# Kernel tuning notes

Measured on AMD Instinct MI355X. Metric: run time of the kernel, lower is better.

Reference implementation:

```python
import jax, jax.numpy as jnp
import numpy as np

B, N0, NCLS = 8, 1024, 40
SPACING, SIGMA_FACTOR = 2.0, 1.0
BLOCKS = [[64, 64], [128, 128], [256, 1024]]
POOL_SIZES = [256, 64, 1]
FC1, FC2 = 512, 256
# 3x3x3 kernel translation grid (27-point support, hard-coded in ConvLayer)
GRID = jnp.asarray(np.array([[i, j, k] for i in (-1, 0, 1) for j in (-1, 0, 1) for k in (-1, 0, 1)], dtype=np.float32))  # [27,3]


def pcnn_conv(pc, feat, W, b, sigma):
    """Extension-operator point convolution.
    pc [B,N,3], feat [B,N,Cin], W [27,Cin,Cout], b [Cout].
    out[b,i,o] = relu( (1/N) * sum_l sum_j exp(-||p_i - p_j + t_l||^2/(2 ks^2)) f[b,j] @ W[l] + b )
    """
    ks = SIGMA_FACTOR * sigma
    trans = SPACING * sigma * GRID                      # [27,3]
    inv = 1.0 / (2.0 * ks * ks)
    diff = pc[:, :, None, :] - pc[:, None, :, :]        # [B,N,N,3]
    d2 = jnp.sum(diff * diff, -1)                       # [B,N,N]
    n = pc.shape[1]

    def body(acc, wt):
        t, Wl = wt                                      # t [3], Wl [Cin,Cout]
        # ||diff + t||^2 = d2 + 2 diff.t + |t|^2
        e = jnp.exp(-(d2 + 2.0 * jnp.einsum('bijd,d->bij', diff, t) + jnp.dot(t, t)) * inv)
        s = jnp.einsum('bij,bjc->bic', e, feat)         # Gaussian-weighted gather
        return acc + jnp.einsum('bic,co->bio', s, Wl), None

    out0 = jnp.zeros((pc.shape[0], n, W.shape[2]), feat.dtype)
    out, _ = jax.lax.scan(body, out0, (trans, W))
    return jax.nn.relu(out / n + b)


def fps(pts, m):
    """Farthest point sampling. pts [N,3] -> indices [m]."""
    d = jnp.sum((pts - pts[0]) ** 2, -1)
    idxs = jnp.zeros((m,), jnp.int32)

    def body(i, state):
        idxs, d = state
        nxt = jnp.argmax(d).astype(jnp.int32)
        idxs = idxs.at[i].set(nxt)
        d = jnp.minimum(d, jnp.sum((pts - pts[nxt]) ** 2, -1))
        return idxs, d

    idxs, _ = jax.lax.fori_loop(1, m, body, (idxs, d))
    return idxs


def pool(pc, feat, m):
    """FPS subsample to m centers, max-pool features over nearest-center clusters."""
    idx = jax.vmap(lambda p: fps(p, m))(pc)                      # [B,m]
    centers = jnp.take_along_axis(pc, idx[..., None], axis=1)    # [B,m,3]
    dist = jnp.sum((pc[:, :, None, :] - centers[:, None, :, :]) ** 2, -1)  # [B,N,m]
    assign = jnp.argmin(dist, -1)                                # [B,N]
    pooled = jax.vmap(lambda f, a: jax.ops.segment_max(f, a, num_segments=m))(feat, assign)
    return centers, pooled


def bn(x, g, b):
    mu = jnp.mean(x, 0)
    v = jnp.var(x, 0)
    return g * (x - mu) * jax.lax.rsqrt(v + 1e-5) + b


def setup_inputs() -> dict:
    key = jax.random.key(0)
    ks = jax.random.split(key, 24)
    inp = {"pc": jax.random.normal(ks[0], (B, 3, N0), jnp.float32)}
    chans = [4, 64, 64, 128, 128, 256, 1024]
    for i, (ci, co) in enumerate(zip(chans[:-1], chans[1:])):
        inp[f"w_c{i}"] = jax.random.normal(ks[1 + i], (27, ci, co), jnp.float32) * 0.05
        inp[f"b_c{i}"] = jnp.zeros((co,), jnp.float32)
    inp["w_fc1"] = jax.random.normal(ks[10], (1024, FC1), jnp.float32) * 0.03
    inp["g_fc1"] = jnp.ones((FC1,), jnp.float32)
    inp["be_fc1"] = jnp.zeros((FC1,), jnp.float32)
    inp["w_fc2"] = jax.random.normal(ks[11], (FC1, FC2), jnp.float32) * 0.05
    inp["g_fc2"] = jnp.ones((FC2,), jnp.float32)
    inp["be_fc2"] = jnp.zeros((FC2,), jnp.float32)
    inp["w_fc3"] = jax.random.normal(ks[12], (FC2, NCLS), jnp.float32) * 0.05
    inp["b_fc3"] = jnp.zeros((NCLS,), jnp.float32)
    return inp


def reference(pc, w_c0, b_c0, w_c1, b_c1, w_c2, b_c2, w_c3, b_c3, w_c4, b_c4, w_c5, b_c5,
              w_fc1, g_fc1, be_fc1, w_fc2, g_fc2, be_fc2, w_fc3, b_fc3):
    pts = jnp.transpose(pc, (0, 2, 1))                           # [B,N,3]
    b_, n0, _ = pts.shape
    feat = jnp.concatenate([pts, jnp.ones((b_, n0, 1), pts.dtype)], -1)  # [B,N,4]
    sigma = 1.0 / float(np.sqrt(n0))  # faithfully uses initial N for all blocks
    ws = [(w_c0, b_c0), (w_c1, b_c1), (w_c2, b_c2), (w_c3, b_c3), (w_c4, b_c4), (w_c5, b_c5)]
    idx = 0
    cur = pts
    for bi, block in enumerate(BLOCKS):
        for _ in block:
            W, bb = ws[idx]
            feat = pcnn_conv(cur, feat, W, bb, sigma)
            idx += 1
        cur, feat = pool(cur, feat, POOL_SIZES[bi])
    x = feat.reshape(b_, -1)                                     # [B,1024]
    x = jax.nn.relu(bn(x @ w_fc1, g_fc1, be_fc1))
    x = jax.nn.relu(bn(x @ w_fc2, g_fc2, be_fc2))
    return x @ w_fc3 + b_fc3
```

## Files before the change

kernel.cpp:

```cpp
#include <hip/hip_runtime.h>
#include <cstdint>
#include <cstddef>
#include <cmath>

constexpr int B = 8;
constexpr int N0 = 1024;
constexpr int CAP = 64;
using u16 = unsigned short;

typedef __bf16 bf16x8 __attribute__((ext_vector_type(8)));
typedef float f32x4 __attribute__((ext_vector_type(4)));

__device__ inline u16 f2bf(float x) {
  unsigned u = __float_as_uint(x);
  return (u16)((u + 0x7fffu + ((u >> 16) & 1u)) >> 16);
}
__device__ inline float bf2f(u16 h) { return __uint_as_float(((unsigned)h) << 16); }
__device__ inline int swk2(int row, int k) {
  int s = (((row >> 2) ^ (row >> 4)) & 3);
  return ((((k >> 3) ^ s) << 3) | (k & 7));
}

__global__ __launch_bounds__(256) void k_prep(const float* __restrict__ pc,
                                              float* __restrict__ pts,
                                              float* __restrict__ feat0,
                                              uint4* __restrict__ p3, int n3,
                                              uint4* __restrict__ p6, int n6,
                                              uint4* __restrict__ p9, int n9) {
  int idx = blockIdx.x * blockDim.x + threadIdx.x;
  if (idx < B * N0) {
    int b = idx / N0, i = idx - b * N0;
    float x = pc[(b * 3 + 0) * N0 + i];
    float y = pc[(b * 3 + 1) * N0 + i];
    float z = pc[(b * 3 + 2) * N0 + i];
    pts[idx * 3 + 0] = x; pts[idx * 3 + 1] = y; pts[idx * 3 + 2] = z;
    feat0[idx * 4 + 0] = x; feat0[idx * 4 + 1] = y; feat0[idx * 4 + 2] = z; feat0[idx * 4 + 3] = 1.0f;
  }
  uint4 v = make_uint4(0xFFFFFFFFu, 0xFFFFFFFFu, 0xFFFFFFFFu, 0xFFFFFFFFu);
  for (int i = idx; i < n3; i += B * N0) p3[i] = v;
  for (int i = idx; i < n6; i += B * N0) p6[i] = v;
  for (int i = idx; i < n9; i += B * N0) p9[i] = v;
}

__global__ __launch_bounds__(256) void k_pairs(const float* __restrict__ pts,
                                               int* __restrict__ pidx, int* __restrict__ pcnt,
                                               int N) {
  const int r = blockIdx.x * 4 + (threadIdx.x >> 6);
  const int lane = threadIdx.x & 63;
  const int b = r / N;
  const float px = pts[(size_t)r * 3 + 0];
  const float py = pts[(size_t)r * 3 + 1];
  const float pz = pts[(size_t)r * 3 + 2];
  int* row = pidx + (size_t)r * CAP;
  int base = 0;
  for (int j0 = 0; j0 < N; j0 += 64) {
    int j = j0 + lane;
    float dx = px - pts[((size_t)b * N + j) * 3 + 0];
    float dy = py - pts[((size_t)b * N + j) * 3 + 1];
    float dz = pz - pts[((size_t)b * N + j) * 3 + 2];
    float d2 = dx * dx + dy * dy + dz * dz;
    bool keep = d2 <= 0.1228f;
    unsigned long long mk = __ballot(keep);
    int pos = __popcll(mk & ((1ull << lane) - 1ull));
    if (keep) { int s = base + pos; if (s < CAP) row[s] = j; }
    base += __popcll(mk);
  }
  if (lane == 0) pcnt[r] = base < CAP ? base : CAP;
}

__global__ void k_econtract(const float* __restrict__ pts, const float* __restrict__ feat,
                            const int* __restrict__ pidx, const int* __restrict__ pcnt,
                            u16* __restrict__ Shi, u16* __restrict__ Slo,
                            int N, int Cin, int K, int Kpad, int mbase) {
  const int g = mbase + blockIdx.x;
  const int b = g / N;
  const int t = threadIdx.x;
  const bool cact = t < Cin;
  const float px = pts[(size_t)g * 3 + 0];
  const float py = pts[(size_t)g * 3 + 1];
  const float pz = pts[(size_t)g * 3 + 2];
  float acc[27];
#pragma unroll
  for (int l = 0; l < 27; ++l) acc[l] = 0.f;
  const int n = pcnt[g];
  const int* row = pidx + (size_t)g * CAP;
  for (int p = 0; p < n; ++p) {
    int j = row[p];
    size_t jb = (size_t)b * N + j;
    float dx = px - pts[jb * 3 + 0];
    float dy = py - pts[jb * 3 + 1];
    float dz = pz - pts[jb * 3 + 2];
    float d2 = dx * dx + dy * dy + dz * dz;
    float base_ = __expf(-512.f * d2);
    float gxv[3] = {__expf(64.f * dx - 2.f), 1.f, __expf(-64.f * dx - 2.f)};
    float gyv[3] = {__expf(64.f * dy - 2.f), 1.f, __expf(-64.f * dy - 2.f)};
    float gzv[3] = {__expf(64.f * dz - 2.f), 1.f, __expf(-64.f * dz - 2.f)};
    float fv = cact ? feat[jb * Cin + t] : 0.f;
#pragma unroll
    for (int a = 0; a < 3; ++a) {
      float ba = base_ * gxv[a];
#pragma unroll
      for (int b2 = 0; b2 < 3; ++b2) {
        float bab = ba * gyv[b2];
#pragma unroll
        for (int c2 = 0; c2 < 3; ++c2) {
          int l = a * 9 + b2 * 3 + c2;
          acc[l] = fmaf(bab * gzv[c2], fv, acc[l]);
        }
      }
    }
  }
  size_t rowo = (size_t)blockIdx.x * Kpad;
  if (cact) {
#pragma unroll
    for (int l = 0; l < 27; ++l) {
      float v = acc[l];
      u16 h = f2bf(v);
      u16 lo = f2bf(v - bf2f(h));
      Shi[rowo + (size_t)l * Cin + t] = h;
      Slo[rowo + (size_t)l * Cin + t] = lo;
    }
  }
  if (Kpad > K && t >= Cin && t < Cin + (Kpad - K)) {
    size_t po = rowo + K + (t - Cin);
    Shi[po] = 0; Slo[po] = 0;
  }
}

__global__ __launch_bounds__(512) void k_gemm_mfma(const u16* __restrict__ Shi,
                                                   const u16* __restrict__ Slo,
                                                   const float* __restrict__ W,
                                                   const float* __restrict__ bias,
                                                   float* __restrict__ out,
                                                   float* __restrict__ P,
                                                   int K, int Kpad, int Cout, float scale,
                                                   int mcur) {
  __shared__ u16 As[2][2][32][40];
  __shared__ u16 Bs[2][2][64][40];
  __shared__ float xch[4][64][8];
  const int t = threadIdx.x;
  const int h = t >> 8;
  const int tl = t & 255;
  const int nb = blockIdx.x * 64;
  const int m0 = blockIdx.y * 32;
  const int l = t & 63, w = t >> 6;
  const int ks = w >> 2, wq = w & 3;
  const int wm = (wq >> 1) * 16, wn = (wq & 1) * 32;
  const int la = l & 15, lg = l >> 4;
  const int ntiles = Kpad >> 6;
  const int KZ = gridDim.z, z = blockIdx.z;
  const int q = ntiles / KZ, r = ntiles % KZ;
  const int t0 = z * q + (z < r ? z : r);
  const int cnt = q + (z < r ? 1 : 0);
  const int ar = tl >> 3, ak = (tl & 7) * 4;
  const size_t aOff = (size_t)(m0 + ar) * Kpad + h * 32 + ak;
  const int aw = swk2(ar, ak);
  const int kp = (tl >> 4) * 2, n4 = (tl & 15) * 4;
  f32x4 acc0 = {0.f, 0.f, 0.f, 0.f}, acc1 = {0.f, 0.f, 0.f, 0.f};

  for (int kt = 0; kt < cnt; ++kt) {
    const int k0 = (t0 + kt) * 64;
    *(ushort4*)&As[h][0][ar][aw] = *(const ushort4*)(Shi + aOff + k0);
    *(ushort4*)&As[h][1][ar][aw] = *(const ushort4*)(Slo + aOff + k0);
    {
      int gk0 = k0 + h * 32 + kp;
      float4 b0 = make_float4(0.f, 0.f, 0.f, 0.f), b1 = b0;
      if (gk0 < K) b0 = *(const float4*)(W + (size_t)gk0 * Cout + nb + n4);
      if (gk0 + 1 < K) b1 = *(const float4*)(W + (size_t)(gk0 + 1) * Cout + nb + n4);
      float v0[4] = {b0.x, b0.y, b0.z, b0.w};
      float v1[4] = {b1.x, b1.y, b1.z, b1.w};
#pragma unroll
      for (int e = 0; e < 4; ++e) {
        int n = n4 + e;
        int kw = swk2(n, kp);
        u16 h0 = f2bf(v0[e]);
        u16 l0 = f2bf(v0[e] - bf2f(h0));
        u16 h1 = f2bf(v1[e]);
        u16 l1 = f2bf(v1[e] - bf2f(h1));
        *(unsigned*)&Bs[h][0][n][kw] = (unsigned)h0 | ((unsigned)h1 << 16);
        *(unsigned*)&Bs[h][1][n][kw] = (unsigned)l0 | ((unsigned)l1 << 16);
      }
    }
    __syncthreads();
    bf16x8 ah = *(const bf16x8*)&As[ks][0][wm + la][swk2(wm + la, lg * 8)];
    bf16x8 al = *(const bf16x8*)&As[ks][1][wm + la][swk2(wm + la, lg * 8)];
    bf16x8 bh0 = *(const bf16x8*)&Bs[ks][0][wn + la][swk2(wn + la, lg * 8)];
    bf16x8 bl0 = *(const bf16x8*)&Bs[ks][1][wn + la][swk2(wn + la, lg * 8)];
    bf16x8 bh1 = *(const bf16x8*)&Bs[ks][0][wn + 16 + la][swk2(wn + 16 + la, lg * 8)];
    bf16x8 bl1 = *(const bf16x8*)&Bs[ks][1][wn + 16 + la][swk2(wn + 16 + la, lg * 8)];
    acc0 = __builtin_amdgcn_mfma_f32_16x16x32_bf16(ah, bh0, acc0, 0, 0, 0);
    acc1 = __builtin_amdgcn_mfma_f32_16x16x32_bf16(ah, bh1, acc1, 0, 0, 0);
    acc0 = __builtin_amdgcn_mfma_f32_16x16x32_bf16(al, bh0, acc0, 0, 0, 0);
    acc1 = __builtin_amdgcn_mfma_f32_16x16x32_bf16(al, bh1, acc1, 0, 0, 0);
    acc0 = __builtin_amdgcn_mfma_f32_16x16x32_bf16(ah, bl0, acc0, 0, 0, 0);
    acc1 = __builtin_amdgcn_mfma_f32_16x16x32_bf16(ah, bl1, acc1, 0, 0, 0);
    __syncthreads();
  }
  if (w >= 4) {
#pragma unroll
    for (int r2 = 0; r2 < 4; ++r2) { xch[wq][l][r2] = acc0[r2]; xch[wq][l][r2 + 4] = acc1[r2]; }
  }
  __syncthreads();
  if (w < 4) {
#pragma unroll
    for (int r2 = 0; r2 < 4; ++r2) { acc0[r2] += xch[wq][l][r2]; acc1[r2] += xch[wq][l][r2 + 4]; }
    if (gridDim.z == 1) {
#pragma unroll
      for (int r2 = 0; r2 < 4; ++r2) {
        int gm = m0 + wm + lg * 4 + r2;
        int gn0 = nb + wn + la;
        out[(size_t)gm * Cout + gn0] = fmaxf(fmaf(acc0[r2], scale, bias[gn0]), 0.f);
        int gn1 = gn0 + 16;
        out[(size_t)gm * Cout + gn1] = fmaxf(fmaf(acc1[r2], scale, bias[gn1]), 0.f);
      }
    } else {
      float* Pz = P + (size_t)z * mcur * Cout;
#pragma unroll
      for (int r2 = 0; r2 < 4; ++r2) {
        int gm = m0 + wm + lg * 4 + r2;
        int gn0 = nb + wn + la;
        Pz[(size_t)gm * Cout + gn0] = acc0[r2];
        Pz[(size_t)gm * Cout + gn0 + 16] = acc1[r2];
      }
    }
  }
}

__global__ __launch_bounds__(256) void k_reduce(const float* __restrict__ P,
                                                const float* __restrict__ bias,
                                                float* __restrict__ out,
                                                int n4, int Cout, int KZ, float scale,
                                                int stride) {
  int i = blockIdx.x * 256 + threadIdx.x;
  if (i >= n4) return;
  float4 s = *(const float4*)(P + (size_t)i * 4);
  for (int z = 1; z < KZ; ++z) {
    float4 v = *(const float4*)(P + (size_t)z * stride + (size_t)i * 4);
    s.x += v.x; s.y += v.y; s.z += v.z; s.w += v.w;
  }
  int c = (i * 4) % Cout;
  float4 bb = *(const float4*)(bias + c);
  float4 o;
  o.x = fmaxf(fmaf(s.x, scale, bb.x), 0.f);
  o.y = fmaxf(fmaf(s.y, scale, bb.y), 0.f);
  o.z = fmaxf(fmaf(s.z, scale, bb.z), 0.f);
  o.w = fmaxf(fmaf(s.w, scale, bb.w), 0.f);
  *(float4*)(out + (size_t)i * 4) = o;
}

template <int CTRL>
__device__ __forceinline__ float dppmaxf(float v) {
  int o = __builtin_amdgcn_update_dpp(0, __float_as_int(v), CTRL, 0xF, 0xF, true);
  return fmaxf(v, __int_as_float(o));
}
__device__ __forceinline__ float wavemaxf(float v) {
  v = dppmaxf<0xB1>(v);
  v = dppmaxf<0x4E>(v);
  v = dppmaxf<0x141>(v);
  v = dppmaxf<0x140>(v);
  v = dppmaxf<0x142>(v);
  v = dppmaxf<0x143>(v);
  return __uint_as_float((unsigned)__builtin_amdgcn_readlane(__float_as_int(v), 63));
}

#define FPS_LOAD(i) \
  float qx##i = src[3 * i + 0], qy##i = src[3 * i + 1], qz##i = src[3 * i + 2];
#define FPS_D0(i) \
  float d##i; { float ax = __fsub_rn(qx##i, x0), ay = __fsub_rn(qy##i, y0), az = __fsub_rn(qz##i, z0); \
    d##i = __fadd_rn(__fadd_rn(__fmul_rn(ax, ax), __fmul_rn(ay, ay)), __fmul_rn(az, az)); }
#define FPS_UPD(i) \
  { float ax = __fsub_rn(qx##i, cx), ay = __fsub_rn(qy##i, cy), az = __fsub_rn(qz##i, cz); \
    float nd = __fadd_rn(__fadd_rn(__fmul_rn(ax, ax), __fmul_rn(ay, ay)), __fmul_rn(az, az)); \
    d##i = fminf(d##i, nd); }
#define FPS_SEL(i) \
  { bool e = (d##i == lbest); sx = e ? qx##i : sx; sy = e ? qy##i : sy; sz = e ? qz##i : sz; }

__global__ __launch_bounds__(64, 1) void k_fps1024(const float* __restrict__ pts,
                                                   float* __restrict__ centers, int m) {
  const int b = blockIdx.x;
  const int t = threadIdx.x;
  const float* P = pts + (size_t)b * 1024 * 3;
  const float* src = P + t * 16 * 3;
  FPS_LOAD(0) FPS_LOAD(1) FPS_LOAD(2) FPS_LOAD(3)
  FPS_LOAD(4) FPS_LOAD(5) FPS_LOAD(6) FPS_LOAD(7)
  FPS_LOAD(8) FPS_LOAD(9) FPS_LOAD(10) FPS_LOAD(11)
  FPS_LOAD(12) FPS_LOAD(13) FPS_LOAD(14) FPS_LOAD(15)
  float x0 = P[0], y0 = P[1], z0 = P[2];
  FPS_D0(0) FPS_D0(1) FPS_D0(2) FPS_D0(3)
  FPS_D0(4) FPS_D0(5) FPS_D0(6) FPS_D0(7)
  FPS_D0(8) FPS_D0(9) FPS_D0(10) FPS_D0(11)
  FPS_D0(12) FPS_D0(13) FPS_D0(14) FPS_D0(15)
  if (t == 0) {
    centers[(size_t)b * m * 3 + 0] = x0;
    centers[(size_t)b * m * 3 + 1] = y0;
    centers[(size_t)b * m * 3 + 2] = z0;
  }
  float lbest;
  {
    float a0 = fmaxf(d0, d1), a1 = fmaxf(d2, d3), a2 = fmaxf(d4, d5), a3 = fmaxf(d6, d7);
    float a4 = fmaxf(d8, d9), a5 = fmaxf(d10, d11), a6 = fmaxf(d12, d13), a7 = fmaxf(d14, d15);
    float b0 = fmaxf(a0, a1), b1 = fmaxf(a2, a3), b2 = fmaxf(a4, a5), b3 = fmaxf(a6, a7);
    lbest = fmaxf(fmaxf(b0, b1), fmaxf(b2, b3));
  }
  for (int it = 1; it < m; ++it) {
    float sx = qx15, sy = qy15, sz = qz15;
    FPS_SEL(14) FPS_SEL(13) FPS_SEL(12) FPS_SEL(11)
    FPS_SEL(10) FPS_SEL(9) FPS_SEL(8) FPS_SEL(7)
    FPS_SEL(6) FPS_SEL(5) FPS_SEL(4) FPS_SEL(3)
    FPS_SEL(2) FPS_SEL(1) FPS_SEL(0)
    float wmax = wavemaxf(lbest);
    unsigned long long mask = __ballot(lbest == wmax);
    int fl = __ffsll((long long)mask) - 1;
    float cx = __uint_as_float((unsigned)__builtin_amdgcn_readlane(__float_as_int(sx), fl));
    float cy = __uint_as_float((unsigned)__builtin_amdgcn_readlane(__float_as_int(sy), fl));
    float cz = __uint_as_float((unsigned)__builtin_amdgcn_readlane(__float_as_int(sz), fl));
    if (t == 0) {
      centers[((size_t)b * m + it) * 3 + 0] = cx;
      centers[((size_t)b * m + it) * 3 + 1] = cy;
      centers[((size_t)b * m + it) * 3 + 2] = cz;
    }
    FPS_UPD(0) FPS_UPD(1) FPS_UPD(2) FPS_UPD(3)
    FPS_UPD(4) FPS_UPD(5) FPS_UPD(6) FPS_UPD(7)
    FPS_UPD(8) FPS_UPD(9) FPS_UPD(10) FPS_UPD(11)
    FPS_UPD(12) FPS_UPD(13) FPS_UPD(14) FPS_UPD(15)
    {
      float a0 = fmaxf(d0, d1), a1 = fmaxf(d2, d3), a2 = fmaxf(d4, d5), a3 = fmaxf(d6, d7);
      float a4 = fmaxf(d8, d9), a5 = fmaxf(d10, d11), a6 = fmaxf(d12, d13), a7 = fmaxf(d14, d15);
      float b0 = fmaxf(a0, a1), b1 = fmaxf(a2, a3), b2 = fmaxf(a4, a5), b3 = fmaxf(a6, a7);
      lbest = fmaxf(fmaxf(b0, b1), fmaxf(b2, b3));
    }
  }
}

__global__ __launch_bounds__(64, 1) void k_fps256(const float* __restrict__ pts,
                                                  float* __restrict__ centers, int m) {
  const int b = blockIdx.x;
  const int t = threadIdx.x;
  const float* P = pts + (size_t)b * 256 * 3;
  const float* src = P + t * 4 * 3;
  FPS_LOAD(0) FPS_LOAD(1) FPS_LOAD(2) FPS_LOAD(3)
  float x0 = P[0], y0 = P[1], z0 = P[2];
  FPS_D0(0) FPS_D0(1) FPS_D0(2) FPS_D0(3)
  if (t == 0) {
    centers[(size_t)b * m * 3 + 0] = x0;
    centers[(size_t)b * m * 3 + 1] = y0;
    centers[(size_t)b * m * 3 + 2] = z0;
  }
  float lbest = fmaxf(fmaxf(d0, d1), fmaxf(d2, d3));
  for (int it = 1; it < m; ++it) {
    float sx = qx3, sy = qy3, sz = qz3;
    FPS_SEL(2) FPS_SEL(1) FPS_SEL(0)
    float wmax = wavemaxf(lbest);
    unsigned long long mask = __ballot(lbest == wmax);
    int fl = __ffsll((long long)mask) - 1;
    float cx = __uint_as_float((unsigned)__builtin_amdgcn_readlane(__float_as_int(sx), fl));
    float cy = __uint_as_float((unsigned)__builtin_amdgcn_readlane(__float_as_int(sy), fl));
    float cz = __uint_as_float((unsigned)__builtin_amdgcn_readlane(__float_as_int(sz), fl));
    if (t == 0) {
      centers[((size_t)b * m + it) * 3 + 0] = cx;
      centers[((size_t)b * m + it) * 3 + 1] = cy;
      centers[((size_t)b * m + it) * 3 + 2] = cz;
    }
    FPS_UPD(0) FPS_UPD(1) FPS_UPD(2) FPS_UPD(3)
    lbest = fmaxf(fmaxf(d0, d1), fmaxf(d2, d3));
  }
}

__global__ __launch_bounds__(64) void k_center0(const float* __restrict__ pts,
                                                float* __restrict__ centers,
                                                int* __restrict__ assign) {
  const int b = blockIdx.x, t = threadIdx.x;
  if (t < 3) centers[b * 3 + t] = pts[(size_t)b * 64 * 3 + t];
  assign[b * 64 + t] = 0;
}

__global__ __launch_bounds__(256) void k_assign(const float* __restrict__ pts,
                                                const float* __restrict__ centers,
                                                int* __restrict__ assign, int N, int m) {
  __shared__ float cs[256 * 3];
  const int t = threadIdx.x;
  const int idx = blockIdx.x * 256 + t;
  const int b = (blockIdx.x * 256) / N;
  for (int i = t; i < m * 3; i += 256) cs[i] = centers[(size_t)b * m * 3 + i];
  __syncthreads();
  float px = pts[(size_t)idx * 3 + 0], py = pts[(size_t)idx * 3 + 1], pz = pts[(size_t)idx * 3 + 2];
  float best = 3.4e38f; int bk = 0;
  for (int k = 0; k < m; ++k) {
    float dx = __fsub_rn(px, cs[k * 3 + 0]);
    float dy = __fsub_rn(py, cs[k * 3 + 1]);
    float dz = __fsub_rn(pz, cs[k * 3 + 2]);
    float dd = __fadd_rn(__fadd_rn(__fmul_rn(dx, dx), __fmul_rn(dy, dy)), __fmul_rn(dz, dz));
    if (dd < best) { best = dd; bk = k; }
  }
  assign[idx] = bk;
}

__global__ __launch_bounds__(256) void k_segmax(const float* __restrict__ feat,
                                                const int* __restrict__ assign,
                                                float* __restrict__ pooled,
                                                int N, int m, int C) {
  int idx = blockIdx.x * blockDim.x + threadIdx.x;
  if (idx >= B * N * C) return;
  int b = idx / (N * C);
  int r = idx - b * N * C;
  int i = r / C;
  int c = r - i * C;
  int a = assign[b * N + i];
  atomicMax((int*)&pooled[((size_t)b * m + a) * C + c], __float_as_int(feat[idx]));
}

template <int K, int COUT, bool BNR>
__global__ __launch_bounds__(256) void k_fc(const float* __restrict__ x,
                                            const float* __restrict__ w,
                                            const float* __restrict__ g,
                                            const float* __restrict__ be,
                                            float* __restrict__ out) {
  __shared__ float ys[8][33];
  int t = threadIdx.x;
  int n = t >> 5, cl = t & 31;
  int c = blockIdx.x * 32 + cl;
  float acc = 0.f;
  if (c < COUT) {
    const float* xr = x + n * K;
    float a0 = 0.f, a1 = 0.f, a2 = 0.f, a3 = 0.f;
    for (int k = 0; k < K; k += 4) {
      a0 = fmaf(xr[k + 0], w[(size_t)(k + 0) * COUT + c], a0);
      a1 = fmaf(xr[k + 1], w[(size_t)(k + 1) * COUT + c], a1);
      a2 = fmaf(xr[k + 2], w[(size_t)(k + 2) * COUT + c], a2);
      a3 = fmaf(xr[k + 3], w[(size_t)(k + 3) * COUT + c], a3);
    }
    acc = (a0 + a1) + (a2 + a3);
  }
  ys[n][cl] = acc;
  __syncthreads();
  if (c >= COUT) return;
  if (BNR) {
    float mu = 0.f;
#pragma unroll
    for (int q = 0; q < 8; ++q) mu += ys[q][cl];
    mu *= 0.125f;
    float var = 0.f;
#pragma unroll
    for (int q = 0; q < 8; ++q) { float dv = ys[q][cl] - mu; var = fmaf(dv, dv, var); }
    var *= 0.125f;
    float rs = 1.f / sqrtf(var + 1e-5f);
    float v = g[c] * (acc - mu) * rs + be[c];
    out[n * COUT + c] = fmaxf(v, 0.f);
  } else {
    out[n * COUT + c] = acc + be[c];
  }
}

extern "C" void kernel_launch(void* const* d_in, const int* in_sizes, int n_in,
                              void* d_out, int out_size, void* d_ws, size_t ws_size,
                              hipStream_t stream) {
  (void)in_sizes; (void)n_in; (void)out_size;
  const float* pc = (const float*)d_in[0];
  const float* Wc[6]; const float* bc[6];
  for (int l = 0; l < 6; ++l) { Wc[l] = (const float*)d_in[1 + 2 * l]; bc[l] = (const float*)d_in[2 + 2 * l]; }
  const float* w1 = (const float*)d_in[13];
  const float* g1 = (const float*)d_in[14];
  const float* be1 = (const float*)d_in[15];
  const float* w2 = (const float*)d_in[16];
  const float* g2 = (const float*)d_in[17];
  const float* be2 = (const float*)d_in[18];
  const float* w3 = (const float*)d_in[19];
  const float* b3 = (const float*)d_in[20];

  float* ws = (float*)d_ws;
  size_t o = 0;
  auto A = [&](size_t n) { size_t r = o; o += (n + 63) & ~(size_t)63; return r; };
  const size_t PTS0 = A((size_t)B * 1024 * 3);
  const size_t PTS1 = A((size_t)B * 256 * 3);
  const size_t PTS2 = A((size_t)B * 64 * 3);
  const size_t PTS3 = A((size_t)B * 3);
  const size_t F0  = A((size_t)B * 1024 * 4);
  const size_t FB1 = A((size_t)B * 1024 * 64);
  const size_t FB2 = A((size_t)B * 1024 * 64);
  const size_t FB3 = A((size_t)B * 256 * 64);
  const size_t FB4 = A((size_t)B * 256 * 128);
  const size_t FB5 = A((size_t)B * 256 * 128);
  const size_t FB6 = A((size_t)B * 64 * 128);
  const size_t FB7 = A((size_t)B * 64 * 256);
  const size_t FB8 = A((size_t)B * 64 * 1024);
  const size_t FB9 = A((size_t)B * 1024);
  const size_t ASSIGN = A((size_t)B * 1024);
  const size_t Y1 = A((size_t)8 * 512);
  const size_t Y2 = A((size_t)8 * 256);
  const size_t PIDX = A((size_t)B * 1024 * CAP);
  const size_t PCNT = A((size_t)B * 1024);
  const size_t dynB = o * sizeof(float);

  int* pidx = (int*)(ws + PIDX);
  int* pcnt = (int*)(ws + PCNT);

  k_prep<<<dim3((B * N0 + 255) / 256), dim3(256), 0, stream>>>(
      pc, ws + PTS0, ws + F0,
      (uint4*)(ws + FB3), B * 256 * 64 / 4,
      (uint4*)(ws + FB6), B * 64 * 128 / 4,
      (uint4*)(ws + FB9), B * 1024 / 4);

  auto conv = [&](size_t ptsOff, size_t finOff, size_t foutOff, int Npts, int Cin, int Cout,
                  const float* W, const float* bias) {
    const int M = B * Npts;
    const int K = 27 * Cin;
    const int Kpad = (K + 63) & ~63;
    const size_t availB = (ws_size > dynB) ? ws_size - dynB : 0;
    size_t pResB = availB / 4;
    if (pResB > (size_t)13 << 20) pResB = (size_t)13 << 20;
    const size_t sByte = availB - pResB;
    long mc = (long)(sByte / ((size_t)Kpad * 4)) & ~31L;
    int Mc = (int)((mc < (long)M) ? mc : (long)M);
    if (Mc < 32) Mc = 32;
    u16* Shi = (u16*)((char*)d_ws + dynB);
    u16* Slo = Shi + (size_t)Mc * Kpad;
    float* P = (float*)(Shi + (size_t)2 * Mc * Kpad);
    const int mch = (M + Mc - 1) / Mc;
    const float scale = 1.f / (float)Npts;
    const int blk = (Cin <= 64) ? 64 : Cin;
    const int ntiles = Kpad >> 6;
    for (int mcb = 0; mcb < mch; ++mcb) {
      const int mb0 = mcb * Mc;
      const int mcur = ((M - mb0) < Mc) ? (M - mb0) : Mc;
      k_econtract<<<dim3(mcur), dim3(blk), 0, stream>>>(ws + ptsOff, ws + finOff, pidx, pcnt,
                                                        Shi, Slo, Npts, Cin, K, Kpad, mb0);
      const int gx = Cout / 64, gy = mcur / 32;
      int kz = 1024 / (gx * gy);
      if (kz < 1) kz = 1;
      if (kz > ntiles) kz = ntiles;
      if (kz > 16) kz = 16;
      long pcap = (long)(pResB / ((size_t)mcur * Cout * 4));
      if ((long)kz > pcap) kz = (pcap < 1) ? 1 : (int)pcap;
      float* outp = ws + foutOff + (size_t)mb0 * Cout;
      k_gemm_mfma<<<dim3(gx, gy, kz), dim3(512), 0, stream>>>(
          Shi, Slo, W, bias, outp, P, K, Kpad, Cout, scale, mcur);
      if (kz > 1) {
        int n4 = mcur * Cout / 4;
        k_reduce<<<dim3((n4 + 255) / 256), dim3(256), 0, stream>>>(
            P, bias, outp, n4, Cout, kz, scale, mcur * Cout);
      }
    }
  };

  k_pairs<<<dim3(B * 1024 / 4), dim3(256), 0, stream>>>(ws + PTS0, pidx, pcnt, 1024);
  conv(PTS0, F0, FB1, 1024, 4, 64, Wc[0], bc[0]);
  conv(PTS0, FB1, FB2, 1024, 64, 64, Wc[1], bc[1]);
  k_fps1024<<<dim3(B), dim3(64), 0, stream>>>(ws + PTS0, ws + PTS1, 256);
  k_assign<<<dim3(B * 1024 / 256), dim3(256), 0, stream>>>(ws + PTS0, ws + PTS1, (int*)(ws + ASSIGN), 1024, 256);
  k_segmax<<<dim3((B * 1024 * 64 + 255) / 256), dim3(256), 0, stream>>>(ws + FB2, (int*)(ws + ASSIGN), ws + FB3, 1024, 256, 64);
  k_pairs<<<dim3(B * 256 / 4), dim3(256), 0, stream>>>(ws + PTS1, pidx, pcnt, 256);
  conv(PTS1, FB3, FB4, 256, 64, 128, Wc[2], bc[2]);
  conv(PTS1, FB4, FB5, 256, 128, 128, Wc[3], bc[3]);
  k_fps256<<<dim3(B), dim3(64), 0, stream>>>(ws + PTS1, ws + PTS2, 64);
  k_assign<<<dim3(B * 256 / 256), dim3(256), 0, stream>>>(ws + PTS1, ws + PTS2, (int*)(ws + ASSIGN), 256, 64);
  k_segmax<<<dim3((B * 256 * 128 + 255) / 256), dim3(256), 0, stream>>>(ws + FB5, (int*)(ws + ASSIGN), ws + FB6, 256, 64, 128);
  k_pairs<<<dim3(B * 64 / 4), dim3(256), 0, stream>>>(ws + PTS2, pidx, pcnt, 64);
  conv(PTS2, FB6, FB7, 64, 128, 256, Wc[4], bc[4]);
  conv(PTS2, FB7, FB8, 64, 256, 1024, Wc[5], bc[5]);
  k_center0<<<dim3(B), dim3(64), 0, stream>>>(ws + PTS2, ws + PTS3, (int*)(ws + ASSIGN));
  k_segmax<<<dim3((B * 64 * 1024 + 255) / 256), dim3(256), 0, stream>>>(ws + FB8, (int*)(ws + ASSIGN), ws + FB9, 64, 1, 1024);
  k_fc<1024, 512, true><<<dim3(512 / 32), dim3(256), 0, stream>>>(ws + FB9, w1, g1, be1, ws + Y1);
  k_fc<512, 256, true><<<dim3(256 / 32), dim3(256), 0, stream>>>(ws + Y1, w2, g2, be2, ws + Y2);
  k_fc<256, 40, false><<<dim3(2), dim3(256), 0, stream>>>(ws + Y2, w3, nullptr, b3, (float*)d_out);
}
```

Measured before the change: 437.8 us.

## Share per-neighbor Gaussian weights via LDS and pack FPS math into pk_f32 ops

In the extension-contraction kernel, lanes 0-26 of each wave now compute one of the 27 translated Gaussian weights directly with a single exp each. The weights go into shared memory, and every channel thread reads them back instead of recomputing 7 exps and the product tree per neighbor. The FPS kernels pair points into float2 vectors and use inline v_pk_add/v_pk_mul to halve the VALU instruction count of the distance update. The exp restructure changes rounding slightly. The LDS exchange relies on a wave-level waitcnt with no barrier, which is only correct because each wave uses its own slot.

```diff
diff --git a/kernel.cpp b/kernel.cpp
--- a/kernel.cpp
+++ b/kernel.cpp
@@ -10,6 +10,7 @@
 
 typedef __bf16 bf16x8 __attribute__((ext_vector_type(8)));
 typedef float f32x4 __attribute__((ext_vector_type(4)));
+typedef float f32x2 __attribute__((ext_vector_type(2)));
 
 __device__ inline u16 f2bf(float x) {
   unsigned u = __float_as_uint(x);
@@ -19,6 +20,12 @@
 __device__ inline int swk2(int row, int k) {
   int s = (((row >> 2) ^ (row >> 4)) & 3);
   return ((((k >> 3) ^ s) << 3) | (k & 7));
+}
+__device__ __forceinline__ f32x2 pkadd(f32x2 a, f32x2 b) {
+  f32x2 d; asm("v_pk_add_f32 %0, %1, %2" : "=v"(d) : "v"(a), "v"(b)); return d;
+}
+__device__ __forceinline__ f32x2 pkmul(f32x2 a, f32x2 b) {
+  f32x2 d; asm("v_pk_mul_f32 %0, %1, %2" : "=v"(d) : "v"(a), "v"(b)); return d;
 }
 
 __global__ __launch_bounds__(256) void k_prep(const float* __restrict__ pc,
@@ -72,13 +79,23 @@
                             const int* __restrict__ pidx, const int* __restrict__ pcnt,
                             u16* __restrict__ Shi, u16* __restrict__ Slo,
                             int N, int Cin, int K, int Kpad, int mbase) {
+  __shared__ float eL[4][28];
   const int g = mbase + blockIdx.x;
   const int b = g / N;
   const int t = threadIdx.x;
+  const int w = t >> 6, lane = t & 63;
   const bool cact = t < Cin;
   const float px = pts[(size_t)g * 3 + 0];
   const float py = pts[(size_t)g * 3 + 1];
   const float pz = pts[(size_t)g * 3 + 2];
+  float sxc = 0.f, syc = 0.f, szc = 0.f, cst = 0.f;
+  if (lane < 27) {
+    int a = lane / 9, bb = (lane / 3) % 3, cc = lane % 3;
+    sxc = (a == 0) ? 64.f : ((a == 2) ? -64.f : 0.f);
+    syc = (bb == 0) ? 64.f : ((bb == 2) ? -64.f : 0.f);
+    szc = (cc == 0) ? 64.f : ((cc == 2) ? -64.f : 0.f);
+    cst = -2.f * (float)((a != 1) + (bb != 1) + (cc != 1));
+  }
   float acc[27];
 #pragma unroll
   for (int l = 0; l < 27; ++l) acc[l] = 0.f;
@@ -91,24 +108,15 @@
     float dy = py - pts[jb * 3 + 1];
     float dz = pz - pts[jb * 3 + 2];
     float d2 = dx * dx + dy * dy + dz * dz;
-    float base_ = __expf(-512.f * d2);
-    float gxv[3] = {__expf(64.f * dx - 2.f), 1.f, __expf(-64.f * dx - 2.f)};
-    float gyv[3] = {__expf(64.f * dy - 2.f), 1.f, __expf(-64.f * dy - 2.f)};
-    float gzv[3] = {__expf(64.f * dz - 2.f), 1.f, __expf(-64.f * dz - 2.f)};
+    if (lane < 27) {
+      float ex = fmaf(-512.f, d2, fmaf(sxc, dx, fmaf(syc, dy, fmaf(szc, dz, cst))));
+      eL[w][lane] = __expf(ex);
+    }
+    asm volatile("s_waitcnt lgkmcnt(0)" ::: "memory");
+    __builtin_amdgcn_sched_barrier(0);
     float fv = cact ? feat[jb * Cin + t] : 0.f;
 #pragma unroll
-    for (int a = 0; a < 3; ++a) {
-      float ba = base_ * gxv[a];
-#pragma unroll
-      for (int b2 = 0; b2 < 3; ++b2) {
-        float bab = ba * gyv[b2];
-#pragma unroll
-        for (int c2 = 0; c2 < 3; ++c2) {
-          int l = a * 9 + b2 * 3 + c2;
-          acc[l] = fmaf(bab * gzv[c2], fv, acc[l]);
-        }
-      }
-    }
+    for (int l = 0; l < 27; ++l) acc[l] = fmaf(eL[w][l], fv, acc[l]);
   }
   size_t rowo = (size_t)blockIdx.x * Kpad;
   if (cact) {
@@ -263,51 +271,51 @@
   return __uint_as_float((unsigned)__builtin_amdgcn_readlane(__float_as_int(v), 63));
 }
 
-#define FPS_LOAD(i) \
-  float qx##i = src[3 * i + 0], qy##i = src[3 * i + 1], qz##i = src[3 * i + 2];
-#define FPS_D0(i) \
-  float d##i; { float ax = __fsub_rn(qx##i, x0), ay = __fsub_rn(qy##i, y0), az = __fsub_rn(qz##i, z0); \
-    d##i = __fadd_rn(__fadd_rn(__fmul_rn(ax, ax), __fmul_rn(ay, ay)), __fmul_rn(az, az)); }
-#define FPS_UPD(i) \
-  { float ax = __fsub_rn(qx##i, cx), ay = __fsub_rn(qy##i, cy), az = __fsub_rn(qz##i, cz); \
-    float nd = __fadd_rn(__fadd_rn(__fmul_rn(ax, ax), __fmul_rn(ay, ay)), __fmul_rn(az, az)); \
-    d##i = fminf(d##i, nd); }
-#define FPS_SEL(i) \
-  { bool e = (d##i == lbest); sx = e ? qx##i : sx; sy = e ? qy##i : sy; sz = e ? qz##i : sz; }
+#define PLOAD(p) \
+  f32x2 X##p = {src[6 * p + 0], src[6 * p + 3]}; \
+  f32x2 Y##p = {src[6 * p + 1], src[6 * p + 4]}; \
+  f32x2 Z##p = {src[6 * p + 2], src[6 * p + 5]};
+#define PPIN(p) asm volatile("" : "+v"(X##p), "+v"(Y##p), "+v"(Z##p));
+#define PD0(p) \
+  f32x2 D##p; { f32x2 ax = pkadd(X##p, n0x), ay = pkadd(Y##p, n0y), az = pkadd(Z##p, n0z); \
+    f32x2 s = pkadd(pkadd(pkmul(ax, ax), pkmul(ay, ay)), pkmul(az, az)); D##p = s; }
+#define PUPD(p) \
+  { f32x2 ax = pkadd(X##p, ncx), ay = pkadd(Y##p, ncy), az = pkadd(Z##p, ncz); \
+    f32x2 s = pkadd(pkadd(pkmul(ax, ax), pkmul(ay, ay)), pkmul(az, az)); \
+    D##p[0] = fminf(D##p[0], s[0]); D##p[1] = fminf(D##p[1], s[1]); }
+#define PSEL(p, hh) \
+  { bool e = (D##p[hh] == lbest); sx = e ? X##p[hh] : sx; sy = e ? Y##p[hh] : sy; sz = e ? Z##p[hh] : sz; }
 
 __global__ __launch_bounds__(64, 1) void k_fps1024(const float* __restrict__ pts,
                                                    float* __restrict__ centers, int m) {
   const int b = blockIdx.x;
   const int t = threadIdx.x;
   const float* P = pts + (size_t)b * 1024 * 3;
-  const float* src = P + t * 16 * 3;
-  FPS_LOAD(0) FPS_LOAD(1) FPS_LOAD(2) FPS_LOAD(3)
-  FPS_LOAD(4) FPS_LOAD(5) FPS_LOAD(6) FPS_LOAD(7)
-  FPS_LOAD(8) FPS_LOAD(9) FPS_LOAD(10) FPS_LOAD(11)
-  FPS_LOAD(12) FPS_LOAD(13) FPS_LOAD(14) FPS_LOAD(15)
+  const float* src = P + t * 48;
+  PLOAD(0) PLOAD(1) PLOAD(2) PLOAD(3) PLOAD(4) PLOAD(5) PLOAD(6) PLOAD(7)
+  PPIN(0) PPIN(1) PPIN(2) PPIN(3) PPIN(4) PPIN(5) PPIN(6) PPIN(7)
   float x0 = P[0], y0 = P[1], z0 = P[2];
-  FPS_D0(0) FPS_D0(1) FPS_D0(2) FPS_D0(3)
-  FPS_D0(4) FPS_D0(5) FPS_D0(6) FPS_D0(7)
-  FPS_D0(8) FPS_D0(9) FPS_D0(10) FPS_D0(11)
-  FPS_D0(12) FPS_D0(13) FPS_D0(14) FPS_D0(15)
+  f32x2 n0x = {-x0, -x0}, n0y = {-y0, -y0}, n0z = {-z0, -z0};
+  PD0(0) PD0(1) PD0(2) PD0(3) PD0(4) PD0(5) PD0(6) PD0(7)
   if (t == 0) {
     centers[(size_t)b * m * 3 + 0] = x0;
     centers[(size_t)b * m * 3 + 1] = y0;
     centers[(size_t)b * m * 3 + 2] = z0;
   }
-  float lbest;
-  {
-    float a0 = fmaxf(d0, d1), a1 = fmaxf(d2, d3), a2 = fmaxf(d4, d5), a3 = fmaxf(d6, d7);
-    float a4 = fmaxf(d8, d9), a5 = fmaxf(d10, d11), a6 = fmaxf(d12, d13), a7 = fmaxf(d14, d15);
-    float b0 = fmaxf(a0, a1), b1 = fmaxf(a2, a3), b2 = fmaxf(a4, a5), b3 = fmaxf(a6, a7);
-    lbest = fmaxf(fmaxf(b0, b1), fmaxf(b2, b3));
-  }
   for (int it = 1; it < m; ++it) {
-    float sx = qx15, sy = qy15, sz = qz15;
-    FPS_SEL(14) FPS_SEL(13) FPS_SEL(12) FPS_SEL(11)
-    FPS_SEL(10) FPS_SEL(9) FPS_SEL(8) FPS_SEL(7)
-    FPS_SEL(6) FPS_SEL(5) FPS_SEL(4) FPS_SEL(3)
-    FPS_SEL(2) FPS_SEL(1) FPS_SEL(0)
+    float lbest;
+    {
+      float m0_ = fmaxf(D0[0], D0[1]), m1 = fmaxf(D1[0], D1[1]);
+      float m2 = fmaxf(D2[0], D2[1]), m3 = fmaxf(D3[0], D3[1]);
+      float m4 = fmaxf(D4[0], D4[1]), m5 = fmaxf(D5[0], D5[1]);
+      float m6 = fmaxf(D6[0], D6[1]), m7 = fmaxf(D7[0], D7[1]);
+      float b0 = fmaxf(m0_, m1), b1 = fmaxf(m2, m3), b2 = fmaxf(m4, m5), b3 = fmaxf(m6, m7);
+      lbest = fmaxf(fmaxf(b0, b1), fmaxf(b2, b3));
+    }
+    float sx = X7[1], sy = Y7[1], sz = Z7[1];
+    PSEL(7, 0) PSEL(6, 1) PSEL(6, 0) PSEL(5, 1) PSEL(5, 0)
+    PSEL(4, 1) PSEL(4, 0) PSEL(3, 1) PSEL(3, 0) PSEL(2, 1)
+    PSEL(2, 0) PSEL(1, 1) PSEL(1, 0) PSEL(0, 1) PSEL(0, 0)
     float wmax = wavemaxf(lbest);
     unsigned long long mask = __ballot(lbest == wmax);
     int fl = __ffsll((long long)mask) - 1;
@@ -319,16 +327,8 @@
       centers[((size_t)b * m + it) * 3 + 1] = cy;
       centers[((size_t)b * m + it) * 3 + 2] = cz;
     }
-    FPS_UPD(0) FPS_UPD(1) FPS_UPD(2) FPS_UPD(3)
-    FPS_UPD(4) FPS_UPD(5) FPS_UPD(6) FPS_UPD(7)
-    FPS_UPD(8) FPS_UPD(9) FPS_UPD(10) FPS_UPD(11)
-    FPS_UPD(12) FPS_UPD(13) FPS_UPD(14) FPS_UPD(15)
-    {
-      float a0 = fmaxf(d0, d1), a1 = fmaxf(d2, d3), a2 = fmaxf(d4, d5), a3 = fmaxf(d6, d7);
-      float a4 = fmaxf(d8, d9), a5 = fmaxf(d10, d11), a6 = fmaxf(d12, d13), a7 = fmaxf(d14, d15);
-      float b0 = fmaxf(a0, a1), b1 = fmaxf(a2, a3), b2 = fmaxf(a4, a5), b3 = fmaxf(a6, a7);
-      lbest = fmaxf(fmaxf(b0, b1), fmaxf(b2, b3));
-    }
+    f32x2 ncx = {-cx, -cx}, ncy = {-cy, -cy}, ncz = {-cz, -cz};
+    PUPD(0) PUPD(1) PUPD(2) PUPD(3) PUPD(4) PUPD(5) PUPD(6) PUPD(7)
   }
 }
 
@@ -337,19 +337,21 @@
   const int b = blockIdx.x;
   const int t = threadIdx.x;
   const float* P = pts + (size_t)b * 256 * 3;
-  const float* src = P + t * 4 * 3;
-  FPS_LOAD(0) FPS_LOAD(1) FPS_LOAD(2) FPS_LOAD(3)
+  const float* src = P + t * 12;
+  PLOAD(0) PLOAD(1)
+  PPIN(0) PPIN(1)
   float x0 = P[0], y0 = P[1], z0 = P[2];
-  FPS_D0(0) FPS_D0(1) FPS_D0(2) FPS_D0(3)
+  f32x2 n0x = {-x0, -x0}, n0y = {-y0, -y0}, n0z = {-z0, -z0};
+  PD0(0) PD0(1)
   if (t == 0) {
     centers[(size_t)b * m * 3 + 0] = x0;
     centers[(size_t)b * m * 3 + 1] = y0;
     centers[(size_t)b * m * 3 + 2] = z0;
   }
-  float lbest = fmaxf(fmaxf(d0, d1), fmaxf(d2, d3));
   for (int it = 1; it < m; ++it) {
-    float sx = qx3, sy = qy3, sz = qz3;
-    FPS_SEL(2) FPS_SEL(1) FPS_SEL(0)
+    float lbest = fmaxf(fmaxf(D0[0], D0[1]), fmaxf(D1[0], D1[1]));
+    float sx = X1[1], sy = Y1[1], sz = Z1[1];
+    PSEL(1, 0) PSEL(0, 1) PSEL(0, 0)
     float wmax = wavemaxf(lbest);
     unsigned long long mask = __ballot(lbest == wmax);
     int fl = __ffsll((long long)mask) - 1;
@@ -361,8 +363,8 @@
       centers[((size_t)b * m + it) * 3 + 1] = cy;
       centers[((size_t)b * m + it) * 3 + 2] = cz;
     }
-    FPS_UPD(0) FPS_UPD(1) FPS_UPD(2) FPS_UPD(3)
-    lbest = fmaxf(fmaxf(d0, d1), fmaxf(d2, d3));
+    f32x2 ncx = {-cx, -cx}, ncy = {-cy, -cy}, ncz = {-cz, -cz};
+    PUPD(0) PUPD(1)
   }
 }
 
```

After: 451.2 us. +3.1%, slower.
